# Performance work log

Measured on AMD Instinct MI355X. Metric: run time of the kernel, lower is better.

The kernel has to match this reference:

```python
import jax, jax.numpy as jnp
import numpy as np

IN_FEATURES = 4096
OUT_FEATURES = 11008
TOKENS = 8192


def setup_inputs() -> dict:
    key = jax.random.key(0)
    k_x, k_w, k_s, k_b = jax.random.split(key, 4)
    x = jax.random.normal(k_x, (TOKENS, IN_FEATURES), dtype=jnp.float32)
    # symmetric int8 weights in [-127, 127]
    qweight = jax.random.randint(k_w, (OUT_FEATURES, IN_FEATURES), -127, 128, dtype=jnp.int32).astype(jnp.int8)
    # per-output-channel positive scale (abs-max / 127 style)
    weight_scale = jax.random.uniform(k_s, (OUT_FEATURES, 1), dtype=jnp.float32, minval=1e-4, maxval=0.02)
    bias = jax.random.normal(k_b, (OUT_FEATURES,), dtype=jnp.float32)
    return {"x": x, "qweight": qweight, "weight_scale": weight_scale, "bias": bias}


def reference(x, qweight, weight_scale, bias):
    # dequantize: [out, in] fp weight = int8 * per-row scale, cast to x dtype
    weight = (qweight.astype(jnp.float32) * weight_scale).astype(x.dtype)
    # F.linear: x @ weight.T + bias
    out = jnp.einsum("ti,oi->to", x, weight) + bias.astype(x.dtype)
    return out
```

## Files before the change

### kernel.cpp

```cpp
#include <hip/hip_runtime.h>
#include <stdint.h>


#define TOKENS 8192
#define IN_F   4096
#define OUT_F  11008

#define BM 256
#define BN 256
#define BK 64
#define KT   (IN_F / BK)
#define MBLK (TOKENS / BM)
#define NBLK (OUT_F / BN)
#define NWG  (MBLK * NBLK)

static_assert(NWG % 8 == 0, "XCD swizzle requires nwg % 8 == 0");
static_assert(KT % 2 == 0, "double-buffer parity");

#define LDS_BUF   32768
#define LDS_TOTAL 65536

typedef __attribute__((ext_vector_type(4))) float f32x4;
typedef __attribute__((ext_vector_type(4))) int   i32x4;

__device__ __forceinline__ void gload_lds16(const void* g, void* l) {
  typedef const __attribute__((address_space(1))) unsigned int* gp_t;
  typedef __attribute__((address_space(3))) unsigned int* lp_t;
  __builtin_amdgcn_global_load_lds((gp_t)g, (lp_t)l, 16, 0, 0);
}

#define MFMA(d, a, b) \
  asm("v_mfma_i32_16x16x64_i8 %0, %1, %2, %0" : "+v"(d) : "v"(a), "v"(b))

#define BARRIER __builtin_amdgcn_s_barrier()
#define LGKM0                                                  \
  do {                                                         \
    asm volatile("s_waitcnt lgkmcnt(0)" ::: "memory");         \
    __builtin_amdgcn_sched_barrier(0);                         \
  } while (0)
#define VMW_(N) asm volatile("s_waitcnt vmcnt(" #N ")" ::: "memory")
#define VMW(N) VMW_(N)
#define PRIO1 __builtin_amdgcn_s_setprio(1)
#define PRIO0 __builtin_amdgcn_s_setprio(0)

__global__ __launch_bounds__(256) void quant_x_kernel(
    const float* __restrict__ x, signed char* __restrict__ xq,
    float* __restrict__ sx) {
  const int row = blockIdx.x;
  const int tid = threadIdx.x;
  const float* xr = x + (size_t)row * IN_F;
  f32x4 v[4];
#pragma unroll
  for (int p = 0; p < 4; ++p) v[p] = ((const f32x4*)xr)[tid + 256 * p];
  float am = 0.f;
#pragma unroll
  for (int p = 0; p < 4; ++p)
#pragma unroll
    for (int j = 0; j < 4; ++j) am = fmaxf(am, fabsf(v[p][j]));
#pragma unroll
  for (int off = 32; off; off >>= 1) am = fmaxf(am, __shfl_xor(am, off, 64));
  __shared__ float wmax[4];
  if ((tid & 63) == 0) wmax[tid >> 6] = am;
  __syncthreads();
  am = fmaxf(fmaxf(wmax[0], wmax[1]), fmaxf(wmax[2], wmax[3]));
  const float inv = (am > 0.f) ? 127.0f / am : 0.f;
  if (tid == 0) sx[row] = (am > 0.f) ? am / 127.0f : 1.0f;
  int* xqi = (int*)(xq + (size_t)row * IN_F);
#pragma unroll
  for (int p = 0; p < 4; ++p) {
    int pk = 0;
#pragma unroll
    for (int j = 0; j < 4; ++j) {
      int q = (int)rintf(v[p][j] * inv);
      pk |= (q & 0xff) << (8 * j);
    }
    xqi[tid + 256 * p] = pk;
  }
}

__global__ void cvt_w_kernel(const int* __restrict__ w,
                             signed char* __restrict__ wq, int n16) {
  int i = blockIdx.x * blockDim.x + threadIdx.x;
  int stride = gridDim.x * blockDim.x;
  for (int c = i; c < n16; c += stride) {
    const i32x4* src = (const i32x4*)w + (size_t)c * 4;
    i32x4 outv;
#pragma unroll
    for (int q = 0; q < 4; ++q) {
      i32x4 v = src[q];
      outv[q] = (v[0] & 0xff) | ((v[1] & 0xff) << 8) |
                ((v[2] & 0xff) << 16) | (v[3] << 24);
    }
    ((i32x4*)wq)[c] = outv;
  }
}

__global__ __launch_bounds__(512) void gemm_i8_kernel(
    const signed char* __restrict__ A,
    const signed char* __restrict__ Bm,
    const float* __restrict__ sx,
    const float* __restrict__ scale,
    const float* __restrict__ bias,
    float* __restrict__ C)
{
  extern __shared__ char lds[];

  const int tid  = threadIdx.x;
  const int lane = tid & 63;
  const int wave = tid >> 6;
  const int wm   = wave >> 2;
  const int wn   = wave & 3;
  const int grp  = lane >> 4;
  const int rsel = lane & 15;

  int bid = blockIdx.x;
  int wg  = (bid & 7) * (NWG / 8) + (bid >> 3);
  const int m_idx = wg % MBLK;
  const int n_idx = wg / MBLK;
  const int row0 = m_idx * BM;
  const int col0 = n_idx * BN;

  const int Lmod  = (tid >> 3) & 7;
  const int slog  = (tid & 7) ^ Lmod;
  const int rreg  = 2 * (tid >> 3) + (slog >> 2);
  const int colOf = (slog & 3) * 16;
  const int gA = (rreg & 63) | ((rreg & 64) << 1);
  const int gB = (rreg & 31) | ((rreg & 96) << 1);
  const signed char* pA0 = A  + (size_t)(row0 + gA) * IN_F + colOf;
  const signed char* pA1 = pA0 + (size_t)64 * IN_F;
  const signed char* pB0 = Bm + (size_t)(col0 + gB) * IN_F + colOf;
  const signed char* pB1 = pB0 + (size_t)32 * IN_F;
  const int stBase = wave * 1024;

  auto stALBL = [&](int bo, int t2) {
    const int ko = t2 * BK;
    gload_lds16(pA0 + ko, lds + bo + 0     + stBase);
    gload_lds16(pB0 + ko, lds + bo + 16384 + stBase);
  };
  auto stBH = [&](int bo, int t2) {
    gload_lds16(pB1 + t2 * BK, lds + bo + 24576 + stBase);
  };
  auto stAH = [&](int bo, int t2) {
    gload_lds16(pA1 + t2 * BK, lds + bo + 8192 + stBase);
  };

  const int sphysR = ((rsel & 1) * 4 + grp) ^ (rsel >> 1);
  const int fOffC  = (rsel >> 1) * 128 + sphysR * 16;
  const int aBase  = wm * 4096 + fOffC;
  const int bBase  = 16384 + wn * 2048 + fOffC;

  i32x4 zero = {0, 0, 0, 0};
  i32x4 acc[8][4];
#pragma unroll
  for (int m = 0; m < 8; ++m)
#pragma unroll
    for (int n = 0; n < 4; ++n) acc[m][n] = zero;

#define DS_A(BO, MI) \
  (*(const i32x4*)(lds + (BO) + ((MI) & 3) * 1024 + ((MI) >> 2) * 8192 + aBase))
#define DS_B(BO, NI) \
  (*(const i32x4*)(lds + (BO) + ((NI) & 1) * 1024 + ((NI) >> 1) * 8192 + bBase))

#define TILE(BO, T, STG, W0, W1, W3)                                           \
  {                                                                            \
    i32x4 arLo[4], arHi[4], brLo[2], brHi[2];                                  \
                                 \
    _Pragma("unroll") for (int m = 0; m < 4; ++m) arLo[m] = DS_A(BO, m);       \
    _Pragma("unroll") for (int n = 0; n < 2; ++n) brLo[n] = DS_B(BO, n);       \
    LGKM0;                                                                     \
    PRIO1;                                                                     \
    _Pragma("unroll") for (int m = 0; m < 4; ++m)                              \
      _Pragma("unroll") for (int n = 0; n < 2; ++n)                            \
        MFMA(acc[m][n], arLo[m], brLo[n]);                                     \
    PRIO0;                                                                     \
    VMW(W0);                                                                   \
    BARRIER;                                                                   \
                        \
    _Pragma("unroll") for (int n = 0; n < 2; ++n) brHi[n] = DS_B(BO, n + 2);   \
    if (STG) stALBL((BO), (T) + 2);                                            \
    LGKM0;                                                                     \
    PRIO1;                                                                     \
    _Pragma("unroll") for (int m = 0; m < 4; ++m)                              \
      _Pragma("unroll") for (int n = 0; n < 2; ++n)                            \
        MFMA(acc[m][n + 2], arLo[m], brHi[n]);                                 \
    PRIO0;                                                                     \
    VMW(W1);                                                                   \
    BARRIER;                                                                   \
                          \
    _Pragma("unroll") for (int m = 0; m < 4; ++m) arHi[m] = DS_A(BO, m + 4);   \
    if (STG) stBH((BO), (T) + 2);                                              \
    LGKM0;                                                                     \
    PRIO1;                                                                     \
    _Pragma("unroll") for (int m = 0; m < 4; ++m)                              \
      _Pragma("unroll") for (int n = 0; n < 2; ++n)                            \
        MFMA(acc[m + 4][n + 2], arHi[m], brHi[n]);                             \
    PRIO0;                                                                     \
    BARRIER;                                                                   \
                      \
    if (STG) stAH((BO), (T) + 2);                                              \
    PRIO1;                                                                     \
    _Pragma("unroll") for (int m = 0; m < 4; ++m)                              \
      _Pragma("unroll") for (int n = 0; n < 2; ++n)                            \
        MFMA(acc[m + 4][n], arHi[m], brLo[n]);                                 \
    PRIO0;                                                                     \
    VMW(W3);                                                                   \
    BARRIER;                                                                   \
  }

  stALBL(0, 0);
  stBH(0, 0);
  stAH(0, 0);
  stALBL(LDS_BUF, 1);
  stBH(LDS_BUF, 1);
  stAH(LDS_BUF, 1);
  VMW(6);
  BARRIER;

  for (int t2 = 0; t2 < KT - 2; t2 += 2) {
    TILE(0,       t2,     true, 5, 6, 6);
    TILE(LDS_BUF, t2 + 1, true, 5, 6, 6);
  }
  TILE(0,       KT - 2, false, 5, 4, 2);
  TILE(LDS_BUF, KT - 1, false, 1, 0, 0);

#undef TILE
#undef DS_A
#undef DS_B

  asm volatile("s_nop 7\n\ts_nop 7" :::);

#pragma unroll
  for (int n = 0; n < 4; ++n) {
    int o = col0 + wn * 64 + n * 16 + rsel;
    float s  = scale[o];
    float bz = bias[o];
#pragma unroll
    for (int m = 0; m < 8; ++m) {
      int tr = row0 + wm * 128 + m * 16 + grp * 4;
      const f32x4 sxv = *(const f32x4*)(sx + tr);
      float* cp = C + (size_t)tr * OUT_F + o;
      i32x4 v = acc[m][n];
      cp[0 * (size_t)OUT_F] = (float)v[0] * (sxv[0] * s) + bz;
      cp[1 * (size_t)OUT_F] = (float)v[1] * (sxv[1] * s) + bz;
      cp[2 * (size_t)OUT_F] = (float)v[2] * (sxv[2] * s) + bz;
      cp[3 * (size_t)OUT_F] = (float)v[3] * (sxv[3] * s) + bz;
    }
  }
}

__global__ void gemm_naive_kernel(const float* __restrict__ x,
                                  const int* __restrict__ w,
                                  const float* __restrict__ sc,
                                  const float* __restrict__ bs,
                                  float* __restrict__ out) {
  long long idx = (long long)blockIdx.x * blockDim.x + threadIdx.x;
  long long total = (long long)TOKENS * OUT_F;
  if (idx >= total) return;
  int t = (int)(idx / OUT_F);
  int o = (int)(idx % OUT_F);
  const float* xp = x + (size_t)t * IN_F;
  const int* wp = w + (size_t)o * IN_F;
  float acc = 0.f;
  for (int k = 0; k < IN_F; k += 4) {
    i32x4 wv = *(const i32x4*)(wp + k);
    f32x4 xv = *(const f32x4*)(xp + k);
    acc += xv[0] * (float)wv[0] + xv[1] * (float)wv[1]
         + xv[2] * (float)wv[2] + xv[3] * (float)wv[3];
  }
  out[idx] = acc * sc[o] + bs[o];
}

extern "C" void kernel_launch(void* const* d_in, const int* in_sizes, int n_in,
                              void* d_out, int out_size, void* d_ws, size_t ws_size,
                              hipStream_t stream) {
  const float* x  = (const float*)d_in[0];
  const int*   qw = (const int*)d_in[1];
  const float* sc = (const float*)d_in[2];
  const float* bs = (const float*)d_in[3];
  float* out = (float*)d_out;

  const size_t xqBytes = (size_t)TOKENS * IN_F;
  const size_t wqBytes = (size_t)OUT_F * IN_F;
  const size_t sxBytes = (size_t)TOKENS * sizeof(float);

  if (ws_size >= xqBytes + wqBytes + sxBytes) {
    signed char* xq = (signed char*)d_ws;
    signed char* wq = (signed char*)((char*)d_ws + xqBytes);
    float*       sx = (float*)((char*)d_ws + xqBytes + wqBytes);
    quant_x_kernel<<<TOKENS, 256, 0, stream>>>(x, xq, sx);
    cvt_w_kernel<<<2048, 256, 0, stream>>>(qw, wq, OUT_F * IN_F / 16);
    (void)hipFuncSetAttribute((const void*)gemm_i8_kernel,
                              hipFuncAttributeMaxDynamicSharedMemorySize,
                              LDS_TOTAL);
    gemm_i8_kernel<<<NWG, 512, LDS_TOTAL, stream>>>(xq, wq, sx, sc, bs, out);
  } else {
    long long total = (long long)TOKENS * OUT_F;
    int blocks = (int)((total + 255) / 256);
    gemm_naive_kernel<<<blocks, 256, 0, stream>>>(x, qw, sc, bs, out);
  }
}
```

Baseline: 570.3 us.

## Halve N tile to 128 and switch to triple-buffered single-barrier K loop

Shrinks the workgroup tile from 256x256 to 256x128, with the 8 waves arranged 4x2 so each owns a 64x64 sub-tile and a 4x4 accumulator set. The four-phase double-buffered schedule becomes a three-buffer ring: each K step issues its 16 MFMAs, prefetches two tiles ahead and uses one barrier. The aim is to double the number of workgroups for a better tail on the last wave, halve accumulator registers so more workgroups can be resident, and cut barriers per K step. The cost is lower arithmetic intensity: more LDS reads per MFMA and more global re-reads of A across N tiles.

```diff
diff --git a/kernel.cpp b/kernel.cpp
--- a/kernel.cpp
+++ b/kernel.cpp
@@ -7,7 +7,7 @@
 #define OUT_F  11008
 
 #define BM 256
-#define BN 256
+#define BN 128
 #define BK 64
 #define KT   (IN_F / BK)
 #define MBLK (TOKENS / BM)
@@ -15,10 +15,9 @@
 #define NWG  (MBLK * NBLK)
 
 static_assert(NWG % 8 == 0, "XCD swizzle requires nwg % 8 == 0");
-static_assert(KT % 2 == 0, "double-buffer parity");
-
-#define LDS_BUF   32768
-#define LDS_TOTAL 65536
+
+#define LDS_BUF   24576
+#define LDS_TOTAL 73728
 
 typedef __attribute__((ext_vector_type(4))) float f32x4;
 typedef __attribute__((ext_vector_type(4))) int   i32x4;
@@ -108,8 +107,8 @@
   const int tid  = threadIdx.x;
   const int lane = tid & 63;
   const int wave = tid >> 6;
-  const int wm   = wave >> 2;
-  const int wn   = wave & 3;
+  const int wm   = wave >> 1;
+  const int wn   = wave & 1;
   const int grp  = lane >> 4;
   const int rsel = lane & 15;
 
@@ -120,110 +119,75 @@
   const int row0 = m_idx * BM;
   const int col0 = n_idx * BN;
 
-  const int Lmod  = (tid >> 3) & 7;
-  const int slog  = (tid & 7) ^ Lmod;
-  const int rreg  = 2 * (tid >> 3) + (slog >> 2);
-  const int colOf = (slog & 3) * 16;
-  const int gA = (rreg & 63) | ((rreg & 64) << 1);
-  const int gB = (rreg & 31) | ((rreg & 96) << 1);
-  const signed char* pA0 = A  + (size_t)(row0 + gA) * IN_F + colOf;
-  const signed char* pA1 = pA0 + (size_t)64 * IN_F;
-  const signed char* pB0 = Bm + (size_t)(col0 + gB) * IN_F + colOf;
-  const signed char* pB1 = pB0 + (size_t)32 * IN_F;
+  const int Lc   = tid >> 3;
+  const int slog = (tid & 7) ^ (Lc & 7);
+  const int rSt  = 2 * Lc + (slog >> 2);
+  const int kSt  = (slog & 3) * 16;
+  const signed char* pA0 = A  + (size_t)(row0 + rSt) * IN_F + kSt;
+  const signed char* pA1 = pA0 + (size_t)128 * IN_F;
+  const signed char* pB0 = Bm + (size_t)(col0 + rSt) * IN_F + kSt;
   const int stBase = wave * 1024;
 
-  auto stALBL = [&](int bo, int t2) {
+  auto stage = [&](int bo, int t2) {
     const int ko = t2 * BK;
     gload_lds16(pA0 + ko, lds + bo + 0     + stBase);
+    gload_lds16(pA1 + ko, lds + bo + 8192  + stBase);
     gload_lds16(pB0 + ko, lds + bo + 16384 + stBase);
   };
-  auto stBH = [&](int bo, int t2) {
-    gload_lds16(pB1 + t2 * BK, lds + bo + 24576 + stBase);
-  };
-  auto stAH = [&](int bo, int t2) {
-    gload_lds16(pA1 + t2 * BK, lds + bo + 8192 + stBase);
-  };
 
   const int sphysR = ((rsel & 1) * 4 + grp) ^ (rsel >> 1);
   const int fOffC  = (rsel >> 1) * 128 + sphysR * 16;
-  const int aBase  = wm * 4096 + fOffC;
-  const int bBase  = 16384 + wn * 2048 + fOffC;
+  const int aOff   = wm * 4096 + fOffC;
+  const int bOff   = 16384 + wn * 4096 + fOffC;
 
   i32x4 zero = {0, 0, 0, 0};
-  i32x4 acc[8][4];
-#pragma unroll
-  for (int m = 0; m < 8; ++m)
+  i32x4 acc[4][4];
+#pragma unroll
+  for (int m = 0; m < 4; ++m)
 #pragma unroll
     for (int n = 0; n < 4; ++n) acc[m][n] = zero;
 
-#define DS_A(BO, MI) \
-  (*(const i32x4*)(lds + (BO) + ((MI) & 3) * 1024 + ((MI) >> 2) * 8192 + aBase))
-#define DS_B(BO, NI) \
-  (*(const i32x4*)(lds + (BO) + ((NI) & 1) * 1024 + ((NI) >> 1) * 8192 + bBase))
-
-#define TILE(BO, T, STG, W0, W1, W3)                                           \
+#define DS_A(BO, MI) (*(const i32x4*)(lds + (BO) + aOff + (MI) * 1024))
+#define DS_B(BO, NI) (*(const i32x4*)(lds + (BO) + bOff + (NI) * 1024))
+
+#define SEG(BO, T, STG, BO2, W)                                                \
   {                                                                            \
-    i32x4 arLo[4], arHi[4], brLo[2], brHi[2];                                  \
-                                 \
-    _Pragma("unroll") for (int m = 0; m < 4; ++m) arLo[m] = DS_A(BO, m);       \
-    _Pragma("unroll") for (int n = 0; n < 2; ++n) brLo[n] = DS_B(BO, n);       \
+    i32x4 ar0 = DS_A(BO, 0), ar1 = DS_A(BO, 1);                                \
+    i32x4 ar2 = DS_A(BO, 2), ar3 = DS_A(BO, 3);                                \
+    i32x4 br0 = DS_B(BO, 0), br1 = DS_B(BO, 1);                                \
+    i32x4 br2 = DS_B(BO, 2), br3 = DS_B(BO, 3);                                \
+    if (STG) stage((BO2), (T) + 2);                                            \
     LGKM0;                                                                     \
     PRIO1;                                                                     \
-    _Pragma("unroll") for (int m = 0; m < 4; ++m)                              \
-      _Pragma("unroll") for (int n = 0; n < 2; ++n)                            \
-        MFMA(acc[m][n], arLo[m], brLo[n]);                                     \
+    MFMA(acc[0][0], ar0, br0); MFMA(acc[0][1], ar0, br1);                      \
+    MFMA(acc[0][2], ar0, br2); MFMA(acc[0][3], ar0, br3);                      \
+    MFMA(acc[1][0], ar1, br0); MFMA(acc[1][1], ar1, br1);                      \
+    MFMA(acc[1][2], ar1, br2); MFMA(acc[1][3], ar1, br3);                      \
+    MFMA(acc[2][0], ar2, br0); MFMA(acc[2][1], ar2, br1);                      \
+    MFMA(acc[2][2], ar2, br2); MFMA(acc[2][3], ar2, br3);                      \
+    MFMA(acc[3][0], ar3, br0); MFMA(acc[3][1], ar3, br1);                      \
+    MFMA(acc[3][2], ar3, br2); MFMA(acc[3][3], ar3, br3);                      \
     PRIO0;                                                                     \
-    VMW(W0);                                                                   \
+    VMW(W);                                                                    \
     BARRIER;                                                                   \
-                        \
-    _Pragma("unroll") for (int n = 0; n < 2; ++n) brHi[n] = DS_B(BO, n + 2);   \
-    if (STG) stALBL((BO), (T) + 2);                                            \
-    LGKM0;                                                                     \
-    PRIO1;                                                                     \
-    _Pragma("unroll") for (int m = 0; m < 4; ++m)                              \
-      _Pragma("unroll") for (int n = 0; n < 2; ++n)                            \
-        MFMA(acc[m][n + 2], arLo[m], brHi[n]);                                 \
-    PRIO0;                                                                     \
-    VMW(W1);                                                                   \
-    BARRIER;                                                                   \
-                          \
-    _Pragma("unroll") for (int m = 0; m < 4; ++m) arHi[m] = DS_A(BO, m + 4);   \
-    if (STG) stBH((BO), (T) + 2);                                              \
-    LGKM0;                                                                     \
-    PRIO1;                                                                     \
-    _Pragma("unroll") for (int m = 0; m < 4; ++m)                              \
-      _Pragma("unroll") for (int n = 0; n < 2; ++n)                            \
-        MFMA(acc[m + 4][n + 2], arHi[m], brHi[n]);                             \
-    PRIO0;                                                                     \
-    BARRIER;                                                                   \
-                      \
-    if (STG) stAH((BO), (T) + 2);                                              \
-    PRIO1;                                                                     \
-    _Pragma("unroll") for (int m = 0; m < 4; ++m)                              \
-      _Pragma("unroll") for (int n = 0; n < 2; ++n)                            \
-        MFMA(acc[m + 4][n], arHi[m], brLo[n]);                                 \
-    PRIO0;                                                                     \
-    VMW(W3);                                                                   \
-    BARRIER;                                                                   \
-  }
-
-  stALBL(0, 0);
-  stBH(0, 0);
-  stAH(0, 0);
-  stALBL(LDS_BUF, 1);
-  stBH(LDS_BUF, 1);
-  stAH(LDS_BUF, 1);
-  VMW(6);
+  }
+
+  stage(0, 0);
+  stage(LDS_BUF, 1);
+  VMW(3);
   BARRIER;
 
-  for (int t2 = 0; t2 < KT - 2; t2 += 2) {
-    TILE(0,       t2,     true, 5, 6, 6);
-    TILE(LDS_BUF, t2 + 1, true, 5, 6, 6);
-  }
-  TILE(0,       KT - 2, false, 5, 4, 2);
-  TILE(LDS_BUF, KT - 1, false, 1, 0, 0);
-
-#undef TILE
+  for (int t = 0; t < 60; t += 3) {
+    SEG(0,           t,     1, 2 * LDS_BUF, 3);
+    SEG(LDS_BUF,     t + 1, 1, 0,           3);
+    SEG(2 * LDS_BUF, t + 2, 1, LDS_BUF,     3);
+  }
+  SEG(0,           60, 1, 2 * LDS_BUF, 3);
+  SEG(LDS_BUF,     61, 1, 0,           3);
+  SEG(2 * LDS_BUF, 62, 0, 0,           0);
+  SEG(0,           63, 0, 0,           0);
+
+#undef SEG
 #undef DS_A
 #undef DS_B
 
@@ -235,8 +199,8 @@
     float s  = scale[o];
     float bz = bias[o];
 #pragma unroll
-    for (int m = 0; m < 8; ++m) {
-      int tr = row0 + wm * 128 + m * 16 + grp * 4;
+    for (int m = 0; m < 4; ++m) {
+      int tr = row0 + wm * 64 + m * 16 + grp * 4;
       const f32x4 sxv = *(const f32x4*)(sx + tr);
       float* cp = C + (size_t)tr * OUT_F + o;
       i32x4 v = acc[m][n];
```

Measured after the change: 652.2 us. 14.4% more time.
